# Kernel optimization log

Hardware: AMD Instinct MI355X
Metric: run time of the kernel (lower is better)

The kernel has to match this reference:

```python
import jax, jax.numpy as jnp
import numpy as np

B, S, H = 1, 2048, 2048
NH, KVH = 32, 8
HD = H // NH
GROUPS = NH // KVH
ROPE_THETA = 10000.0


def _rope(x):
    # x: (b, s, heads, head_dim); HF-style rotate-half RoPE
    d = x.shape[-1]
    s = x.shape[1]
    inv_freq = 1.0 / (ROPE_THETA ** (jnp.arange(0, d, 2, dtype=jnp.float32) / d))
    t = jnp.arange(s, dtype=jnp.float32)
    freqs = jnp.einsum('s,f->sf', t, inv_freq)          # (s, d/2)
    emb = jnp.concatenate([freqs, freqs], axis=-1)       # (s, d)
    cos = jnp.cos(emb)[None, :, None, :].astype(x.dtype)
    sin = jnp.sin(emb)[None, :, None, :].astype(x.dtype)
    x1, x2 = x[..., : d // 2], x[..., d // 2:]
    rot = jnp.concatenate([-x2, x1], axis=-1)
    return x * cos + rot * sin


def setup_inputs() -> dict:
    key = jax.random.key(0)
    ks = jax.random.split(key, 6)
    scale = 0.02
    hidden_states = jax.random.normal(ks[0], (B, S, H), dtype=jnp.float32)
    Wq = jax.random.normal(ks[1], (H, NH, HD), dtype=jnp.float32) * scale
    Wk = jax.random.normal(ks[2], (H, KVH, HD), dtype=jnp.float32) * scale
    Wv = jax.random.normal(ks[3], (H, KVH, HD), dtype=jnp.float32) * scale
    Wo = jax.random.normal(ks[4], (H, H), dtype=jnp.float32) * scale
    # causal additive mask (b,1,s,s): 0 on/below diagonal, large negative above
    causal = jnp.tril(jnp.ones((S, S), dtype=bool))
    attention_mask = jnp.where(causal, 0.0, -1e9).astype(jnp.float32)[None, None]
    return {"hidden_states": hidden_states, "Wq": Wq, "Wk": Wk, "Wv": Wv,
            "Wo": Wo, "attention_mask": attention_mask}


def reference(hidden_states, Wq, Wk, Wv, Wo, attention_mask):
    b, s, _ = hidden_states.shape
    q = jnp.einsum('bsh,hnd->bsnd', hidden_states, Wq)   # (b,s,NH,HD)
    k = jnp.einsum('bsh,hnd->bsnd', hidden_states, Wk)   # (b,s,KVH,HD)
    v = jnp.einsum('bsh,hnd->bsnd', hidden_states, Wv)   # (b,s,KVH,HD)
    q = _rope(q)
    k = _rope(k)
    # GQA: tile kv heads along head axis (tf.tile semantics)
    k = jnp.tile(k, (1, 1, GROUPS, 1))                   # (b,s,NH,HD)
    v = jnp.tile(v, (1, 1, GROUPS, 1))
    # scores: 'aecd,abcd->acbe' -> (b, heads, q_len, k_len)
    scores = jnp.einsum('bend,bqnd->bnqe', k, q) / jnp.sqrt(
        jnp.asarray(HD, dtype=q.dtype))
    scores = scores + attention_mask
    scores = jnp.maximum(scores, jnp.finfo(scores.dtype).min)
    probs = jax.nn.softmax(scores, axis=-1)
    attn = jnp.einsum('bnqe,bend->bqnd', probs, v)       # (b,s,NH,HD)
    attn = attn.reshape(b, s, H)
    return jnp.einsum('bsh,hd->bsd', attn, Wo)
```

## Files before the change

### kernel.cpp

```cpp
#include <hip/hip_runtime.h>
#include <stdint.h>

typedef unsigned short u16;
typedef uint32_t u32;
typedef uint64_t u64;
typedef float f32x4 __attribute__((ext_vector_type(4)));
typedef float f32x16 __attribute__((ext_vector_type(16)));
typedef __bf16 bf16x8 __attribute__((ext_vector_type(8)));

#define S_LEN 2048
#define HID 2048
#define N_HEADS 32
#define KV_HEADS 8
#define HEAD_DIM 64
#define QKV_COLS 3072

__device__ __forceinline__ u16 f2b(float x) {
  union { float f; uint32_t u; } c; c.f = x;
  uint32_t u = (c.u + 0x7fffu + ((c.u >> 16) & 1u)) >> 16;
  return (u16)u;
}
__device__ __forceinline__ float b2f(u16 v) {
  union { uint32_t u; float f; } c; c.u = ((uint32_t)v) << 16;
  return c.f;
}
__device__ __forceinline__ u32 pkbf(float e, float o) {
  union { float f; u32 u; } a, b; a.f = e; b.f = o;
  return __builtin_amdgcn_perm(b.u, a.u, 0x07060302u);
}

#define GLL16(gptr, lptr)                                                      \
  __builtin_amdgcn_global_load_lds(                                            \
      (__attribute__((address_space(1))) void*)(gptr),                         \
      (__attribute__((address_space(3))) void*)(lptr), 16, 0, 0)

__global__ void cvt_f32_bf16(const float* __restrict__ in, u16* __restrict__ out, int n4) {
  int i = blockIdx.x * blockDim.x + threadIdx.x;
  if (i >= n4) return;
  float4 v = reinterpret_cast<const float4*>(in)[i];
  ushort4 o;
  o.x = f2b(v.x); o.y = f2b(v.y); o.z = f2b(v.z); o.w = f2b(v.w);
  reinterpret_cast<ushort4*>(out)[i] = o;
}

__global__ void transpose_f32_bf16(const float* __restrict__ in, u16* __restrict__ out,
                                   int R, int C) {
  __shared__ float tile[32][33];
  int c0 = blockIdx.x * 32, r0 = blockIdx.y * 32;
  int tx = threadIdx.x, ty = threadIdx.y;
#pragma unroll
  for (int i = 0; i < 32; i += 8)
    tile[ty + i][tx] = in[(size_t)(r0 + ty + i) * C + c0 + tx];
  __syncthreads();
#pragma unroll
  for (int i = 0; i < 32; i += 8)
    out[(size_t)(c0 + ty + i) * R + r0 + tx] = f2b(tile[tx][ty + i]);
}

__global__ void transpose_bf16(const u16* __restrict__ in, int istride,
                               u16* __restrict__ out, int R, int C) {
  __shared__ u16 tile[32][33];
  int c0 = blockIdx.x * 32, r0 = blockIdx.y * 32;
  int tx = threadIdx.x, ty = threadIdx.y;
#pragma unroll
  for (int i = 0; i < 32; i += 8)
    tile[ty + i][tx] = in[(size_t)(r0 + ty + i) * istride + c0 + tx];
  __syncthreads();
#pragma unroll
  for (int i = 0; i < 32; i += 8)
    out[(size_t)(c0 + ty + i) * R + r0 + tx] = tile[tx][ty + i];
}

__global__ void rope_kernel(u16* __restrict__ x, int lognh, int rowStride, float scale) {
  int idx = blockIdx.x * blockDim.x + threadIdx.x;
  int i = idx & 31;
  int h = (idx >> 5) & ((1 << lognh) - 1);
  int s = idx >> (5 + lognh);
  u16* p = x + (size_t)s * rowStride + h * HEAD_DIM;
  float inv = __expf(-(float)i * (9.210340371976184f / 32.0f));
  float f = (float)s * inv;
  float sn, cs;
  sincosf(f, &sn, &cs);
  float x1 = b2f(p[i]), x2 = b2f(p[i + 32]);
  p[i]      = f2b((x1 * cs - x2 * sn) * scale);
  p[i + 32] = f2b((x2 * cs + x1 * sn) * scale);
}

template <bool OUTF32>
__global__ __launch_bounds__(256) void gemm128(const u16* __restrict__ A,
                                               const u16* __restrict__ BT,
                                               void* __restrict__ Cp,
                                               int M, int N, int K) {
  __shared__ __align__(16) u16 As[128 * 64];
  __shared__ __align__(16) u16 Bs[128 * 64];
  const int t = threadIdx.x;
  const int w = t >> 6, l = t & 63;
  const int lr = l & 15, lk = l >> 4;
  const int wr = w >> 1, wc = w & 1;
  const int m0 = blockIdx.x * 128, n0 = blockIdx.y * 128;

  f32x4 acc[4][4];
#pragma unroll
  for (int m = 0; m < 4; ++m)
#pragma unroll
    for (int n = 0; n < 4; ++n)
      acc[m][n] = (f32x4){0.f, 0.f, 0.f, 0.f};

  const u16* aSrc = A + (size_t)(m0 + t / 8) * K + (t % 8) * 8;
  const u16* bSrc = BT + (size_t)(n0 + t / 8) * K + (t % 8) * 8;
  char* aDst = (char*)As + w * 1024;
  char* bDst = (char*)Bs + w * 1024;

  for (int k0 = 0; k0 < K; k0 += 64) {
#pragma unroll
    for (int i = 0; i < 4; ++i)
      GLL16(aSrc + (size_t)i * 32 * K + k0, aDst + i * 4096);
#pragma unroll
    for (int i = 0; i < 4; ++i)
      GLL16(bSrc + (size_t)i * 32 * K + k0, bDst + i * 4096);
    __syncthreads();
#pragma unroll
    for (int kk = 0; kk < 2; ++kk) {
      bf16x8 af[4], bfr[4];
#pragma unroll
      for (int m = 0; m < 4; ++m)
        af[m] = *(const bf16x8*)&As[(wr * 64 + m * 16 + lr) * 64 + kk * 32 + lk * 8];
#pragma unroll
      for (int n = 0; n < 4; ++n)
        bfr[n] = *(const bf16x8*)&Bs[(wc * 64 + n * 16 + lr) * 64 + kk * 32 + lk * 8];
#pragma unroll
      for (int m = 0; m < 4; ++m)
#pragma unroll
        for (int n = 0; n < 4; ++n)
          acc[m][n] = __builtin_amdgcn_mfma_f32_16x16x32_bf16(af[m], bfr[n], acc[m][n], 0, 0, 0);
    }
    __syncthreads();
  }
#pragma unroll
  for (int m = 0; m < 4; ++m)
#pragma unroll
    for (int n = 0; n < 4; ++n) {
      int row0 = m0 + wr * 64 + m * 16 + lk * 4;
      int col = n0 + wc * 64 + n * 16 + lr;
#pragma unroll
      for (int r = 0; r < 4; ++r) {
        if constexpr (OUTF32)
          ((float*)Cp)[(size_t)(row0 + r) * N + col] = acc[m][n][r];
        else
          ((u16*)Cp)[(size_t)(row0 + r) * N + col] = f2b(acc[m][n][r]);
      }
    }
}

__global__ __launch_bounds__(256) void attn_kernel(const u16* __restrict__ QKV,
                                                   const u16* __restrict__ Vt,
                                                   u16* __restrict__ At) {
  __shared__ __align__(16) u16 scratch[4][32 * 64];
  const int t = threadIdx.x;
  const int w = t >> 6, l = t & 63;
  const int lq = l & 31;
  const int hi = l >> 5;
  const int b = blockIdx.x;
  const int qt = (b < 256) ? (63 - (b >> 3)) : ((b - 256) >> 3);
  const int head = (b & 7) * 4 + w;
  const int kvh = head & (KV_HEADS - 1);
  const int qbase = qt * 32;
  char* pb = (char*)scratch[w];
  const int swrow = lq * 128;
  const int swx = (lq & 7) << 4;

  bf16x8 qf[4];
  {
    const u16* qp = QKV + (size_t)(qbase + lq) * QKV_COLS + head * HEAD_DIM + hi * 8;
#pragma unroll
    for (int jj = 0; jj < 4; ++jj) qf[jj] = *(const bf16x8*)(qp + jj * 16);
  }
  const u16* Kb = QKV + HID + kvh * HEAD_DIM;
  const u16* Vb = Vt + (size_t)(kvh * HEAD_DIM) * S_LEN;

  f32x16 oacc0, oacc1;
#pragma unroll
  for (int i = 0; i < 16; ++i) { oacc0[i] = 0.f; oacc1[i] = 0.f; }
  float m_run = -1e30f;
  float l_run = 0.f;

  auto process = [&](int kv0, bool mask0, bool mask1) {
    const u16* kp = Kb + (size_t)(kv0 + lq) * QKV_COLS + hi * 8;
    bf16x8 kf0[4], kf1[4];
#pragma unroll
    for (int jj = 0; jj < 4; ++jj) {
      kf0[jj] = *(const bf16x8*)(kp + jj * 16);
      kf1[jj] = *(const bf16x8*)(kp + (size_t)32 * QKV_COLS + jj * 16);
    }
    f32x16 s0, s1;
#pragma unroll
    for (int i = 0; i < 16; ++i) { s0[i] = 0.f; s1[i] = 0.f; }
#pragma unroll
    for (int jj = 0; jj < 4; ++jj)
      s0 = __builtin_amdgcn_mfma_f32_32x32x16_bf16(kf0[jj], qf[jj], s0, 0, 0, 0);
#pragma unroll
    for (int jj = 0; jj < 4; ++jj)
      s1 = __builtin_amdgcn_mfma_f32_32x32x16_bf16(kf1[jj], qf[jj], s1, 0, 0, 0);
    bf16x8 vf0[4], vf1[4];
    const u16* vp = Vb + (size_t)lq * S_LEN + kv0 + hi * 8;
#pragma unroll
    for (int ks = 0; ks < 4; ++ks) {
      vf0[ks] = *(const bf16x8*)(vp + ks * 16);
      vf1[ks] = *(const bf16x8*)(vp + (size_t)32 * S_LEN + ks * 16);
    }
    if (mask0) {
      const int c = kv0 - qbase;
#pragma unroll
      for (int r = 0; r < 16; ++r) {
        int kvr = (r & 3) + 8 * (r >> 2) + 4 * hi + c;
        s0[r] = (kvr > lq) ? -1e30f : s0[r];
      }
    }
    if (mask1) {
      const int c = kv0 + 32 - qbase;
#pragma unroll
      for (int r = 0; r < 16; ++r) {
        int kvr = (r & 3) + 8 * (r >> 2) + 4 * hi + c;
        s1[r] = (kvr > lq) ? -1e30f : s1[r];
      }
    }
    float mx[16];
#pragma unroll
    for (int r = 0; r < 16; ++r) mx[r] = fmaxf(s0[r], s1[r]);
#pragma unroll
    for (int st = 8; st >= 1; st >>= 1)
#pragma unroll
      for (int r = 0; r < st; ++r) mx[r] = fmaxf(mx[r], mx[r + st]);
    float pm = mx[0];
    pm = fmaxf(pm, __shfl_xor(pm, 32));
    if (!__all(pm <= m_run + 8.f)) {
      float mnew = fmaxf(m_run, pm);
      float esc = exp2f(m_run - mnew);
      m_run = mnew;
      l_run *= esc;
#pragma unroll
      for (int i = 0; i < 16; ++i) { oacc0[i] *= esc; oacc1[i] *= esc; }
    }
#pragma unroll
    for (int r = 0; r < 16; ++r) {
      s0[r] = exp2f(s0[r] - m_run);
      s1[r] = exp2f(s1[r] - m_run);
    }
    float ls[16];
#pragma unroll
    for (int r = 0; r < 16; ++r) ls[r] = s0[r] + s1[r];
#pragma unroll
    for (int st = 8; st >= 1; st >>= 1)
#pragma unroll
      for (int r = 0; r < st; ++r) ls[r] += ls[r + st];
    l_run += ls[0];
#pragma unroll
    for (int sb = 0; sb < 2; ++sb)
#pragma unroll
      for (int g = 0; g < 4; ++g) {
        u32 w0 = sb ? pkbf(s1[4 * g + 0], s1[4 * g + 1]) : pkbf(s0[4 * g + 0], s0[4 * g + 1]);
        u32 w1 = sb ? pkbf(s1[4 * g + 2], s1[4 * g + 3]) : pkbf(s0[4 * g + 2], s0[4 * g + 3]);
        int kvb2 = (32 * sb + 8 * g + 4 * hi) * 2;
        *(u64*)(pb + swrow + (kvb2 ^ swx)) = (u64)w0 | ((u64)w1 << 32);
      }
    asm volatile("s_waitcnt lgkmcnt(0)" ::: "memory");
    __builtin_amdgcn_sched_barrier(0);
    bf16x8 pa[4];
#pragma unroll
    for (int ks = 0; ks < 4; ++ks)
      pa[ks] = *(const bf16x8*)(pb + swrow + ((32 * ks + 16 * hi) ^ swx));
    asm volatile("" ::: "memory");
#pragma unroll
    for (int ks = 0; ks < 4; ++ks) {
      oacc0 = __builtin_amdgcn_mfma_f32_32x32x16_bf16(vf0[ks], pa[ks], oacc0, 0, 0, 0);
      oacc1 = __builtin_amdgcn_mfma_f32_32x32x16_bf16(vf1[ks], pa[ks], oacc1, 0, 0, 0);
    }
  };

  const int NTF = qt >> 1;
  for (int tl = 0; tl < NTF; ++tl) process(tl * 64, false, false);
  process(NTF * 64, (qt & 1) == 0, true);

  float l_tot = l_run + __shfl_xor(l_run, 32);
  float inv = 1.0f / l_tot;
  asm volatile("" ::: "memory");
#pragma unroll
  for (int dt = 0; dt < 2; ++dt) {
#pragma unroll
    for (int j = 0; j < 8; ++j) {
      int d = dt * 32 + 2 * (j & 1) + 8 * (j >> 1) + 4 * hi;
      float e = (dt ? oacc1[2 * j] : oacc0[2 * j]) * inv;
      float o = (dt ? oacc1[2 * j + 1] : oacc0[2 * j + 1]) * inv;
      *(u32*)(pb + swrow + ((d * 2) ^ swx)) = pkbf(e, o);
    }
  }
  asm volatile("s_waitcnt lgkmcnt(0)" ::: "memory");
  __builtin_amdgcn_sched_barrier(0);
#pragma unroll
  for (int pass = 0; pass < 4; ++pass) {
    int qq = pass * 8 + (l >> 3);
    int coff = (l & 7) * 16;
    f32x4 v = *(const f32x4*)(pb + qq * 128 + (coff ^ ((qq & 7) << 4)));
    *(f32x4*)&At[(size_t)(qbase + qq) * HID + head * HEAD_DIM + (l & 7) * 8] = v;
  }
}

extern "C" void kernel_launch(void* const* d_in, const int* in_sizes, int n_in,
                              void* d_out, int out_size, void* d_ws, size_t ws_size,
                              hipStream_t stream) {
  const float* hs = (const float*)d_in[0];
  const float* Wq = (const float*)d_in[1];
  const float* Wk = (const float*)d_in[2];
  const float* Wv = (const float*)d_in[3];
  const float* Wo = (const float*)d_in[4];

  char* ws = (char*)d_ws;
  const size_t MB = 1024 * 1024;
  u16* X     = (u16*)(ws + 0 * MB);
  u16* WqkvT = (u16*)(ws + 8 * MB);
  u16* WoT   = (u16*)(ws + 20 * MB);
  u16* QKV   = (u16*)(ws + 28 * MB);
  u16* Vt    = (u16*)(ws + 40 * MB);
  u16* At    = (u16*)(ws + 42 * MB);

  cvt_f32_bf16<<<(S_LEN * HID / 4 + 255) / 256, 256, 0, stream>>>(hs, X, S_LEN * HID / 4);
  transpose_f32_bf16<<<dim3(64, 64), dim3(32, 8), 0, stream>>>(Wq, WqkvT, 2048, 2048);
  transpose_f32_bf16<<<dim3(16, 64), dim3(32, 8), 0, stream>>>(Wk, WqkvT + 2048 * 2048, 2048, 512);
  transpose_f32_bf16<<<dim3(16, 64), dim3(32, 8), 0, stream>>>(Wv, WqkvT + 2048 * 2048 + 512 * 2048, 2048, 512);
  transpose_f32_bf16<<<dim3(64, 64), dim3(32, 8), 0, stream>>>(Wo, WoT, 2048, 2048);
  gemm128<false><<<dim3(16, 24), 256, 0, stream>>>(X, WqkvT, QKV, 2048, QKV_COLS, 2048);
  rope_kernel<<<(S_LEN * N_HEADS * 32) / 256, 256, 0, stream>>>(QKV, 5, QKV_COLS, 0.18033688011112042f);
  rope_kernel<<<(S_LEN * KV_HEADS * 32) / 256, 256, 0, stream>>>(QKV + HID, 3, QKV_COLS, 1.0f);
  transpose_bf16<<<dim3(16, 64), dim3(32, 8), 0, stream>>>(QKV + HID + 512, QKV_COLS, Vt, 2048, 512);
  attn_kernel<<<dim3(512), 256, 0, stream>>>(QKV, Vt, At);
  gemm128<true><<<dim3(16, 16), 256, 0, stream>>>(At, WoT, (float*)d_out, 2048, 2048, 2048);
}
```

Baseline: 308.4 us.

## Fuse prep kernels, split-K GEMMs with fused RoPE reduction, prefetch K in attention

Merges the input conversion and four weight transposes into one launch. Both GEMMs now use split-K of two, writing fp32 partials; a new post kernel sums the partials and applies RoPE, scaling and the bf16 cast, replacing the separate rope kernels. A final kernel sums the output partials. The attention loop double-buffers K tile loads so the next tile's loads are issued before the current tile is computed. The cost is extra fp32 partial traffic and additional reduction kernels.

```diff
diff --git a/kernel.cpp b/kernel.cpp
--- a/kernel.cpp
+++ b/kernel.cpp
@@ -14,6 +14,7 @@
 #define KV_HEADS 8
 #define HEAD_DIM 64
 #define QKV_COLS 3072
+#define QSCALE 0.18033688011112042f
 
 __device__ __forceinline__ u16 f2b(float x) {
   union { float f; uint32_t u; } c; c.f = x;
@@ -34,27 +35,41 @@
       (__attribute__((address_space(1))) void*)(gptr),                         \
       (__attribute__((address_space(3))) void*)(lptr), 16, 0, 0)
 
-__global__ void cvt_f32_bf16(const float* __restrict__ in, u16* __restrict__ out, int n4) {
-  int i = blockIdx.x * blockDim.x + threadIdx.x;
-  if (i >= n4) return;
-  float4 v = reinterpret_cast<const float4*>(in)[i];
-  ushort4 o;
-  o.x = f2b(v.x); o.y = f2b(v.y); o.z = f2b(v.z); o.w = f2b(v.w);
-  reinterpret_cast<ushort4*>(out)[i] = o;
-}
-
-__global__ void transpose_f32_bf16(const float* __restrict__ in, u16* __restrict__ out,
-                                   int R, int C) {
-  __shared__ float tile[32][33];
-  int c0 = blockIdx.x * 32, r0 = blockIdx.y * 32;
-  int tx = threadIdx.x, ty = threadIdx.y;
-#pragma unroll
-  for (int i = 0; i < 32; i += 8)
-    tile[ty + i][tx] = in[(size_t)(r0 + ty + i) * C + c0 + tx];
-  __syncthreads();
-#pragma unroll
-  for (int i = 0; i < 32; i += 8)
-    out[(size_t)(c0 + ty + i) * R + r0 + tx] = f2b(tile[tx][ty + i]);
+__global__ __launch_bounds__(256) void prep_fused(const float* __restrict__ Wq,
+                                                  const float* __restrict__ Wk,
+                                                  const float* __restrict__ Wv,
+                                                  const float* __restrict__ Wo,
+                                                  const float* __restrict__ hs,
+                                                  u16* __restrict__ WqkvT,
+                                                  u16* __restrict__ WoT,
+                                                  u16* __restrict__ X) {
+  const int b = blockIdx.x;
+  const int t = threadIdx.x;
+  if (b < 10240) {
+    __shared__ float tile[32][33];
+    const float* in;
+    u16* out;
+    int C, bx, by;
+    if (b < 4096) { in = Wq; out = WqkvT; C = 2048; bx = b & 63; by = b >> 6; }
+    else if (b < 5120) { int bb = b - 4096; in = Wk; out = WqkvT + 2048 * 2048; C = 512; bx = bb & 15; by = bb >> 4; }
+    else if (b < 6144) { int bb = b - 5120; in = Wv; out = WqkvT + 2048 * 2048 + 512 * 2048; C = 512; bx = bb & 15; by = bb >> 4; }
+    else { int bb = b - 6144; in = Wo; out = WoT; C = 2048; bx = bb & 63; by = bb >> 6; }
+    const int tx = t & 31, ty = t >> 5;
+    const int c0 = bx * 32, r0 = by * 32;
+#pragma unroll
+    for (int i = 0; i < 32; i += 8)
+      tile[ty + i][tx] = in[(size_t)(r0 + ty + i) * C + c0 + tx];
+    __syncthreads();
+#pragma unroll
+    for (int i = 0; i < 32; i += 8)
+      out[(size_t)(c0 + ty + i) * 2048 + r0 + tx] = f2b(tile[tx][ty + i]);
+  } else {
+    int i = (b - 10240) * 256 + t;
+    float4 v = reinterpret_cast<const float4*>(hs)[i];
+    ushort4 o;
+    o.x = f2b(v.x); o.y = f2b(v.y); o.z = f2b(v.z); o.w = f2b(v.w);
+    reinterpret_cast<ushort4*>(X)[i] = o;
+  }
 }
 
 __global__ void transpose_bf16(const u16* __restrict__ in, int istride,
@@ -71,26 +86,10 @@
     out[(size_t)(c0 + ty + i) * R + r0 + tx] = tile[tx][ty + i];
 }
 
-__global__ void rope_kernel(u16* __restrict__ x, int lognh, int rowStride, float scale) {
-  int idx = blockIdx.x * blockDim.x + threadIdx.x;
-  int i = idx & 31;
-  int h = (idx >> 5) & ((1 << lognh) - 1);
-  int s = idx >> (5 + lognh);
-  u16* p = x + (size_t)s * rowStride + h * HEAD_DIM;
-  float inv = __expf(-(float)i * (9.210340371976184f / 32.0f));
-  float f = (float)s * inv;
-  float sn, cs;
-  sincosf(f, &sn, &cs);
-  float x1 = b2f(p[i]), x2 = b2f(p[i + 32]);
-  p[i]      = f2b((x1 * cs - x2 * sn) * scale);
-  p[i + 32] = f2b((x2 * cs + x1 * sn) * scale);
-}
-
-template <bool OUTF32>
-__global__ __launch_bounds__(256) void gemm128(const u16* __restrict__ A,
-                                               const u16* __restrict__ BT,
-                                               void* __restrict__ Cp,
-                                               int M, int N, int K) {
+__global__ __launch_bounds__(256) void gemm128s(const u16* __restrict__ A,
+                                                const u16* __restrict__ BT,
+                                                float* __restrict__ Cp,
+                                                int M, int N, int K, int ksplit) {
   __shared__ __align__(16) u16 As[128 * 64];
   __shared__ __align__(16) u16 Bs[128 * 64];
   const int t = threadIdx.x;
@@ -98,6 +97,10 @@
   const int lr = l & 15, lk = l >> 4;
   const int wr = w >> 1, wc = w & 1;
   const int m0 = blockIdx.x * 128, n0 = blockIdx.y * 128;
+  const int z = blockIdx.z;
+  const int kspan = K / ksplit;
+  const int kBeg = z * kspan, kEnd = kBeg + kspan;
+  Cp += (size_t)z * M * N;
 
   f32x4 acc[4][4];
 #pragma unroll
@@ -111,7 +114,7 @@
   char* aDst = (char*)As + w * 1024;
   char* bDst = (char*)Bs + w * 1024;
 
-  for (int k0 = 0; k0 < K; k0 += 64) {
+  for (int k0 = kBeg; k0 < kEnd; k0 += 64) {
 #pragma unroll
     for (int i = 0; i < 4; ++i)
       GLL16(aSrc + (size_t)i * 32 * K + k0, aDst + i * 4096);
@@ -143,13 +146,46 @@
       int row0 = m0 + wr * 64 + m * 16 + lk * 4;
       int col = n0 + wc * 64 + n * 16 + lr;
 #pragma unroll
-      for (int r = 0; r < 4; ++r) {
-        if constexpr (OUTF32)
-          ((float*)Cp)[(size_t)(row0 + r) * N + col] = acc[m][n][r];
-        else
-          ((u16*)Cp)[(size_t)(row0 + r) * N + col] = f2b(acc[m][n][r]);
-      }
-    }
+      for (int r = 0; r < 4; ++r)
+        Cp[(size_t)(row0 + r) * N + col] = acc[m][n][r];
+    }
+}
+
+__global__ __launch_bounds__(256) void post_qkv(const float* __restrict__ P0,
+                                                const float* __restrict__ P1,
+                                                u16* __restrict__ QKV) {
+  int idx = blockIdx.x * 256 + threadIdx.x;
+  int s = idx / 1536, j = idx - s * 1536;
+  const float* r0 = P0 + (size_t)s * QKV_COLS;
+  const float* r1 = P1 + (size_t)s * QKV_COLS;
+  u16* o = QKV + (size_t)s * QKV_COLS;
+  if (j < 1280) {
+    int hbase, i;
+    float scale;
+    if (j < 1024) { hbase = (j >> 5) * 64; i = j & 31; scale = QSCALE; }
+    else { int jj = j - 1024; hbase = 2048 + (jj >> 5) * 64; i = jj & 31; scale = 1.0f; }
+    int c1 = hbase + i, c2 = c1 + 32;
+    float inv = __expf(-(float)i * (9.210340371976184f / 32.0f));
+    float f = (float)s * inv;
+    float sn, cs;
+    sincosf(f, &sn, &cs);
+    float x1 = r0[c1] + r1[c1], x2 = r0[c2] + r1[c2];
+    o[c1] = f2b((x1 * cs - x2 * sn) * scale);
+    o[c2] = f2b((x2 * cs + x1 * sn) * scale);
+  } else {
+    int c = 2560 + (j - 1280) * 2;
+    *(u32*)(o + c) = pkbf(r0[c] + r1[c], r0[c + 1] + r1[c + 1]);
+  }
+}
+
+__global__ __launch_bounds__(256) void post_out(const float* __restrict__ P0,
+                                                const float* __restrict__ P1,
+                                                float* __restrict__ out) {
+  int i = blockIdx.x * 256 + threadIdx.x;
+  float4 a = reinterpret_cast<const float4*>(P0)[i];
+  float4 b = reinterpret_cast<const float4*>(P1)[i];
+  a.x += b.x; a.y += b.y; a.z += b.z; a.w += b.w;
+  reinterpret_cast<float4*>(out)[i] = a;
 }
 
 __global__ __launch_bounds__(256) void attn_kernel(const u16* __restrict__ QKV,
@@ -184,14 +220,16 @@
   float m_run = -1e30f;
   float l_run = 0.f;
 
-  auto process = [&](int kv0, bool mask0, bool mask1) {
+  auto loadK = [&](int kv0, bf16x8* k0, bf16x8* k1) {
     const u16* kp = Kb + (size_t)(kv0 + lq) * QKV_COLS + hi * 8;
-    bf16x8 kf0[4], kf1[4];
 #pragma unroll
     for (int jj = 0; jj < 4; ++jj) {
-      kf0[jj] = *(const bf16x8*)(kp + jj * 16);
-      kf1[jj] = *(const bf16x8*)(kp + (size_t)32 * QKV_COLS + jj * 16);
-    }
+      k0[jj] = *(const bf16x8*)(kp + jj * 16);
+      k1[jj] = *(const bf16x8*)(kp + (size_t)32 * QKV_COLS + jj * 16);
+    }
+  };
+
+  auto tile = [&](int kv0, const bf16x8* kf0, const bf16x8* kf1, bool mask0, bool mask1) {
     f32x16 s0, s1;
 #pragma unroll
     for (int i = 0; i < 16; ++i) { s0[i] = 0.f; s1[i] = 0.f; }
@@ -278,8 +316,22 @@
   };
 
   const int NTF = qt >> 1;
-  for (int tl = 0; tl < NTF; ++tl) process(tl * 64, false, false);
-  process(NTF * 64, (qt & 1) == 0, true);
+  bf16x8 ka0[4], ka1[4], kb0[4], kb1[4];
+  loadK(0, ka0, ka1);
+  int tl = 0;
+  for (; tl + 2 <= NTF; tl += 2) {
+    loadK((tl + 1) * 64, kb0, kb1);
+    tile(tl * 64, ka0, ka1, false, false);
+    loadK((tl + 2) * 64, ka0, ka1);
+    tile((tl + 1) * 64, kb0, kb1, false, false);
+  }
+  if (tl < NTF) {
+    loadK((tl + 1) * 64, kb0, kb1);
+    tile(tl * 64, ka0, ka1, false, false);
+    tile(NTF * 64, kb0, kb1, (qt & 1) == 0, true);
+  } else {
+    tile(NTF * 64, ka0, ka1, (qt & 1) == 0, true);
+  }
 
   float l_tot = l_run + __shfl_xor(l_run, 32);
   float inv = 1.0f / l_tot;
@@ -316,22 +368,20 @@
 
   char* ws = (char*)d_ws;
   const size_t MB = 1024 * 1024;
-  u16* X     = (u16*)(ws + 0 * MB);
-  u16* WqkvT = (u16*)(ws + 8 * MB);
-  u16* WoT   = (u16*)(ws + 20 * MB);
-  u16* QKV   = (u16*)(ws + 28 * MB);
-  u16* Vt    = (u16*)(ws + 40 * MB);
-  u16* At    = (u16*)(ws + 42 * MB);
-
-  cvt_f32_bf16<<<(S_LEN * HID / 4 + 255) / 256, 256, 0, stream>>>(hs, X, S_LEN * HID / 4);
-  transpose_f32_bf16<<<dim3(64, 64), dim3(32, 8), 0, stream>>>(Wq, WqkvT, 2048, 2048);
-  transpose_f32_bf16<<<dim3(16, 64), dim3(32, 8), 0, stream>>>(Wk, WqkvT + 2048 * 2048, 2048, 512);
-  transpose_f32_bf16<<<dim3(16, 64), dim3(32, 8), 0, stream>>>(Wv, WqkvT + 2048 * 2048 + 512 * 2048, 2048, 512);
-  transpose_f32_bf16<<<dim3(64, 64), dim3(32, 8), 0, stream>>>(Wo, WoT, 2048, 2048);
-  gemm128<false><<<dim3(16, 24), 256, 0, stream>>>(X, WqkvT, QKV, 2048, QKV_COLS, 2048);
-  rope_kernel<<<(S_LEN * N_HEADS * 32) / 256, 256, 0, stream>>>(QKV, 5, QKV_COLS, 0.18033688011112042f);
-  rope_kernel<<<(S_LEN * KV_HEADS * 32) / 256, 256, 0, stream>>>(QKV + HID, 3, QKV_COLS, 1.0f);
+  u16* X      = (u16*)(ws + 0 * MB);
+  u16* WqkvT  = (u16*)(ws + 8 * MB);
+  u16* WoT    = (u16*)(ws + 20 * MB);
+  u16* QKV    = (u16*)(ws + 28 * MB);
+  u16* Vt     = (u16*)(ws + 40 * MB);
+  u16* At     = (u16*)(ws + 42 * MB);
+  float* QKVp = (float*)(ws + 50 * MB);
+  float* Op   = (float*)(ws + 50 * MB);
+
+  prep_fused<<<14336, 256, 0, stream>>>(Wq, Wk, Wv, Wo, hs, WqkvT, WoT, X);
+  gemm128s<<<dim3(16, 24, 2), 256, 0, stream>>>(X, WqkvT, QKVp, 2048, QKV_COLS, 2048, 2);
+  post_qkv<<<12288, 256, 0, stream>>>(QKVp, QKVp + (size_t)2048 * QKV_COLS, QKV);
   transpose_bf16<<<dim3(16, 64), dim3(32, 8), 0, stream>>>(QKV + HID + 512, QKV_COLS, Vt, 2048, 512);
   attn_kernel<<<dim3(512), 256, 0, stream>>>(QKV, Vt, At);
-  gemm128<true><<<dim3(16, 16), 256, 0, stream>>>(At, WoT, (float*)d_out, 2048, 2048, 2048);
-}
+  gemm128s<<<dim3(16, 16, 2), 256, 0, stream>>>(At, WoT, Op, 2048, 2048, 2048, 2);
+  post_out<<<4096, 256, 0, stream>>>(Op, Op + (size_t)2048 * 2048, (float*)d_out);
+}
```

New measurement: 293.0 us. -5.0%, faster.
